# Optimization experiments

Hardware: AMD Instinct MI355X
Metric: run time of the kernel (lower is better)

Reference implementation:

```python
import jax, jax.numpy as jnp
import numpy as np

# Profile-HMM forward-backward in log space.
# inputs : (M, B, L, S) soft/one-hot observation features
# log_A  : (M, Q, Q) row-stochastic log transition matrix
# log_pi : (M, Q)    log initial distribution
# log_B  : (M, Q, S) log emission matrix

M, B, L, Q, S = 1, 64, 2048, 256, 26
EPS = 1e-16


def setup_inputs() -> dict:
    key = jax.random.key(0)
    k1, k2, k3, k4 = jax.random.split(key, 4)
    inputs = jax.random.uniform(k1, (M, B, L, S), dtype=jnp.float32)
    log_A = jax.nn.log_softmax(jax.random.normal(k2, (M, Q, Q), dtype=jnp.float32), axis=-1)
    log_pi = jax.nn.log_softmax(jax.random.normal(k3, (M, Q), dtype=jnp.float32), axis=-1)
    log_B = jax.nn.log_softmax(jax.random.normal(k4, (M, Q, S), dtype=jnp.float32), axis=-1)
    return {"inputs": inputs, "log_A": log_A, "log_pi": log_pi, "log_B": log_B}


def _forward_backward(inputs, log_A, log_pi, log_B):
    # emission probs per state: e[m,b,l,q] = sum_s inputs[m,b,l,s] * B[m,q,s]
    emit = jnp.einsum('mbls,mqs->mblq', inputs, jnp.exp(log_B))
    log_e = jnp.log(emit + EPS)
    log_e_t = jnp.moveaxis(log_e, 2, 0)  # (L, M, B, Q) time-major

    # forward recursion: alpha_t[i] = logsumexp_j(alpha_{t-1}[j] + A[j,i]) + e_t[i]
    alpha0 = log_pi[:, None, :] + log_e_t[0]  # (M, B, Q)

    def fstep(alpha, le):
        new = jax.nn.logsumexp(alpha[..., :, None] + log_A[:, None], axis=-2) + le
        return new, new

    _, alphas = jax.lax.scan(fstep, alpha0, log_e_t[1:])
    alphas = jnp.concatenate([alpha0[None], alphas], axis=0)  # (L, M, B, Q)

    # backward recursion: beta_t[i] = logsumexp_j(A[i,j] + e_{t+1}[j] + beta_{t+1}[j])
    beta_last = jnp.zeros_like(alpha0)

    def bstep(beta, le):
        new = jax.nn.logsumexp(log_A[:, None] + (le + beta)[:, :, None, :], axis=-1)
        return new, new

    _, betas = jax.lax.scan(bstep, beta_last, log_e_t[1:], reverse=True)
    betas = jnp.concatenate([betas, beta_last[None]], axis=0)  # (L, M, B, Q)

    loglik = jax.nn.logsumexp(alphas[-1], axis=-1)  # (M, B)
    post = alphas + betas - loglik[None, :, :, None]  # state posterior log probs
    return jnp.moveaxis(post, 0, 2), loglik  # (M, B, L, Q), (M, B)


def reference(inputs, log_A, log_pi, log_B):
    post, loglik = _forward_backward(inputs, log_A, log_pi, log_B)
    return post, loglik
```

## Files before the change

kernel.cpp:

```cpp
#include <hip/hip_runtime.h>

namespace {

constexpr int B = 64;
constexpr int L = 2048;
constexpr int Q = 256;
constexpr int S = 26;
constexpr float EPS = 1e-16f;
constexpr size_t POST = (size_t)B * L * Q;

typedef _Float16 f16x8 __attribute__((ext_vector_type(8)));
typedef float f32x4 __attribute__((ext_vector_type(4)));

#define MFMA16(a, b, c) __builtin_amdgcn_mfma_f32_16x16x32_f16((a), (b), (c), 0, 0, 0)

struct Smem {
  alignas(16) _Float16 vb[2][Q];
  float sh[2];
  alignas(16) float afin[Q];
};

__device__ __forceinline__ void lds_barrier() {
  asm volatile("s_waitcnt lgkmcnt(0)\n\ts_barrier" ::: "memory");
}

__device__ __forceinline__ float wave_max64(float x) {
#pragma unroll
  for (int off = 32; off > 0; off >>= 1) x = fmaxf(x, __shfl_xor(x, off, 64));
  return x;
}
__device__ __forceinline__ float wave_sum64(float x) {
#pragma unroll
  for (int off = 32; off > 0; off >>= 1) x += __shfl_xor(x, off, 64);
  return x;
}

__device__ __forceinline__ void load_emit_frags(const float* __restrict__ log_B,
                                                int c0, int c1, int g, int q,
                                                f16x8& Bh0, f16x8& Bl0,
                                                f16x8& Bh1, f16x8& Bl1) {
#pragma unroll
  for (int j = 0; j < 8; ++j) {
    const int s = g * 8 + j;
    const float v0 = (s < S) ? __expf(log_B[(size_t)(c0 + q) * S + s]) : 0.f;
    const float v1 = (s < S) ? __expf(log_B[(size_t)(c1 + q) * S + s]) : 0.f;
    const _Float16 h0 = (_Float16)v0, h1 = (_Float16)v1;
    Bh0[j] = h0; Bl0[j] = (_Float16)(v0 - (float)h0);
    Bh1[j] = h1; Bl1[j] = (_Float16)(v1 - (float)h1);
  }
}

__device__ __forceinline__ void load_row(const float* __restrict__ row, int g,
                                         bool rdl, float2* ld) {
  if (rdl) {
    const float2* r2 = (const float2*)(row + g * 8);
    ld[0] = r2[0];
    if (g < 3) { ld[1] = r2[1]; ld[2] = r2[2]; ld[3] = r2[3]; }
  }
}

__device__ __forceinline__ void cvt_row(const float2* ld, f16x8& xh, f16x8& xl) {
#pragma unroll
  for (int i = 0; i < 4; ++i) {
    const float a = ld[i].x, bb = ld[i].y;
    const _Float16 ah = (_Float16)a, bh = (_Float16)bb;
    xh[2 * i] = ah;     xl[2 * i] = (_Float16)(a - (float)ah);
    xh[2 * i + 1] = bh; xl[2 * i + 1] = (_Float16)(bb - (float)bh);
  }
}

__device__ __forceinline__ void emit_mfma(const f16x8& xh, const f16x8& xl,
                                          const f16x8& Bh0, const f16x8& Bl0,
                                          const f16x8& Bh1, const f16x8& Bl1,
                                          f32x4& E0, f32x4& E1) {
  const f32x4 Z = {0.f, 0.f, 0.f, 0.f};
  E0 = MFMA16(xh, Bl0, Z);
  E0 = MFMA16(xl, Bh0, E0);
  E0 = MFMA16(xh, Bh0, E0);
  E1 = MFMA16(xh, Bl1, Z);
  E1 = MFMA16(xl, Bh1, E1);
  E1 = MFMA16(xh, Bh1, E1);
}

__device__ __forceinline__ void matvec_mfma(const f16x8* va, const f16x8* T0,
                                            const f16x8* T1, float& x0, float& x1) {
  const f32x4 Z = {0.f, 0.f, 0.f, 0.f};
  f32x4 X0a = MFMA16(va[0], T0[0], Z);
  f32x4 X1a = MFMA16(va[0], T1[0], Z);
  f32x4 X0b = MFMA16(va[4], T0[4], Z);
  f32x4 X1b = MFMA16(va[4], T1[4], Z);
#pragma unroll
  for (int f = 1; f < 4; ++f) {
    X0a = MFMA16(va[f], T0[f], X0a);
    X1a = MFMA16(va[f], T1[f], X1a);
    X0b = MFMA16(va[f + 4], T0[f + 4], X0b);
    X1b = MFMA16(va[f + 4], T1[f + 4], X1b);
  }
  x0 = X0a[0] + X0b[0];
  x1 = X1a[0] + X1b[0];
}

__device__ __forceinline__ void read_frags(Smem& sm, int p, int g, f16x8* va) {
  const _Float16* vbp = sm.vb[p];
#pragma unroll
  for (int f = 0; f < 8; ++f) va[f] = *(const f16x8*)(vbp + f * 32 + g * 8);
}

__device__ __forceinline__ void fwd_impl(int b, const float* __restrict__ inputs,
                                         const float* __restrict__ log_A,
                                         const float* __restrict__ log_pi,
                                         const float* __restrict__ log_B,
                                         float* __restrict__ out, Smem& sm) {
  const int tid = threadIdx.x, w = tid >> 6, lane = tid & 63;
  const int g = lane >> 4, q = lane & 15;
  const int c0 = w * 32, c1 = c0 + 16;
  const bool rdl = (q == 0);
  const bool epi = (lane < 16);

  f16x8 T0[8], T1[8];
#pragma unroll
  for (int f = 0; f < 8; ++f) {
#pragma unroll
    for (int j = 0; j < 8; ++j) {
      const int k = f * 32 + g * 8 + j;
      T0[f][j] = (_Float16)__expf(log_A[(size_t)k * Q + c0 + q]);
      T1[f][j] = (_Float16)__expf(log_A[(size_t)k * Q + c1 + q]);
    }
  }
  f16x8 Bh0, Bl0, Bh1, Bl1;
  load_emit_frags(log_B, c0, c1, g, q, Bh0, Bl0, Bh1, Bl1);

  const float* __restrict__ rowbase = inputs + (size_t)b * L * S;
  float* __restrict__ post_b = out + (size_t)b * L * Q;

  float2 ld[4] = {{0.f, 0.f}, {0.f, 0.f}, {0.f, 0.f}, {0.f, 0.f}};
  f16x8 xh = {}, xl = {};
  f16x8 va[8];
#pragma unroll
  for (int f = 0; f < 8; ++f) va[f] = f16x8{};

  load_row(rowbase, g, rdl, ld);
  cvt_row(ld, xh, xl);
  f32x4 E0, E1;
  emit_mfma(xh, xl, Bh0, Bl0, Bh1, Bl1, E0, E1);
  load_row(rowbase + S, g, rdl, ld);
  float zh0 = 1.f, zh1 = 1.f, rdp_h = 0.f;
  if (epi) {
    zh0 = (E0[0] + EPS) * __expf(log_pi[c0 + lane]);
    zh1 = (E1[0] + EPS) * __expf(log_pi[c1 + lane]);
  }
  if (tid == 0) sm.sh[0] = __logf(zh0);
  lds_barrier();
  float rd_prev = sm.sh[0];
  if (epi) {
    const float sc = __expf(-rd_prev);
    sm.vb[0][c0 + lane] = (_Float16)(zh0 * sc);
    sm.vb[0][c1 + lane] = (_Float16)(zh1 * sc);
  }
  lds_barrier();

  int p = 0;
  for (int t = 1; t < L; ++t) {
    const float rd = sm.sh[p];
    if (rdl) read_frags(sm, p, g, va);
    cvt_row(ld, xh, xl);
    const int tt = (t + 1 < L) ? t + 1 : L - 1;
    load_row(rowbase + (size_t)tt * S, g, rdl, ld);
    if (epi) {
      const float a0 = __logf(zh0) + rdp_h;
      const float a1 = __logf(zh1) + rdp_h;
      post_b[(size_t)(t - 1) * Q + c0 + lane] = a0;
      post_b[(size_t)(t - 1) * Q + c1 + lane] = a1;
    }
    f32x4 E0_, E1_;
    emit_mfma(xh, xl, Bh0, Bl0, Bh1, Bl1, E0_, E1_);
    float x0, x1;
    matvec_mfma(va, T0, T1, x0, x1);
    const float gam = __expf(rd_prev - rd);
    if (epi) {
      const float e0 = E0_[0] + EPS, e1 = E1_[0] + EPS;
      const float z0 = x0 * e0, z1 = x1 * e1;
      sm.vb[p ^ 1][c0 + lane] = (_Float16)(z0 * gam);
      sm.vb[p ^ 1][c1 + lane] = (_Float16)(z1 * gam);
      if (tid == 0) sm.sh[p ^ 1] = __logf(z0) + rd_prev;
      zh0 = z0; zh1 = z1;
    }
    rdp_h = rd_prev;
    rd_prev = rd;
    lds_barrier();
    p ^= 1;
  }

  if (epi) {
    const float a0 = __logf(zh0) + rdp_h;
    const float a1 = __logf(zh1) + rdp_h;
    post_b[(size_t)(L - 1) * Q + c0 + lane] = a0;
    post_b[(size_t)(L - 1) * Q + c1 + lane] = a1;
    sm.afin[c0 + lane] = a0;
    sm.afin[c1 + lane] = a1;
  }
  lds_barrier();
  if (w == 0) {
    float4 fa = ((const float4*)sm.afin)[lane];
    float m = fmaxf(fmaxf(fa.x, fa.y), fmaxf(fa.z, fa.w));
    m = wave_max64(m);
    float ss = __expf(fa.x - m) + __expf(fa.y - m) + __expf(fa.z - m) + __expf(fa.w - m);
    ss = wave_sum64(ss);
    if (lane == 0) out[POST + b] = __logf(ss) + m;
  }
}

template <int MODE>
__device__ __forceinline__ void bwd_impl(int b, const float* __restrict__ inputs,
                                         const float* __restrict__ log_A,
                                         const float* __restrict__ log_B,
                                         float* __restrict__ out,
                                         float* __restrict__ ws, Smem& sm) {
  const int tid = threadIdx.x, w = tid >> 6, lane = tid & 63;
  const int g = lane >> 4, q = lane & 15;
  const int c0 = w * 32, c1 = c0 + 16;
  const bool rdl = (q == 0);
  const bool epi = (lane < 16);

  f16x8 T0[8], T1[8];
#pragma unroll
  for (int f = 0; f < 8; ++f) {
#pragma unroll
    for (int j = 0; j < 8; ++j) {
      const int k = f * 32 + g * 8 + j;
      T0[f][j] = (_Float16)__expf(log_A[(size_t)(c0 + q) * Q + k]);
      T1[f][j] = (_Float16)__expf(log_A[(size_t)(c1 + q) * Q + k]);
    }
  }
  f16x8 Bh0, Bl0, Bh1, Bl1;
  load_emit_frags(log_B, c0, c1, g, q, Bh0, Bl0, Bh1, Bl1);

  const float* __restrict__ rowbase = inputs + (size_t)b * L * S;
  float* __restrict__ post_b = out + (size_t)b * L * Q;
  float* __restrict__ ws_b = ws + (size_t)b * L * Q;

  float ll = 0.f, a_h0 = 0.f, a_h1 = 0.f;
  if (MODE == 1) {
    ll = out[POST + b];
    if (epi) {
      a_h0 = post_b[(size_t)(L - 1) * Q + c0 + lane];
      a_h1 = post_b[(size_t)(L - 1) * Q + c1 + lane];
    }
  }

  float2 ld[4] = {{0.f, 0.f}, {0.f, 0.f}, {0.f, 0.f}, {0.f, 0.f}};
  f16x8 xh = {}, xl = {};
  f16x8 va[8];
#pragma unroll
  for (int f = 0; f < 8; ++f) va[f] = f16x8{};

  load_row(rowbase + (size_t)(L - 1) * S, g, rdl, ld);
  cvt_row(ld, xh, xl);
  f32x4 E0, E1;
  emit_mfma(xh, xl, Bh0, Bl0, Bh1, Bl1, E0, E1);
  load_row(rowbase + (size_t)(L - 2) * S, g, rdl, ld);
  float e0i = 1.f, e1i = 1.f;
  if (epi) { e0i = E0[0] + EPS; e1i = E1[0] + EPS; }
  if (tid == 0) sm.sh[0] = __logf(e0i);
  lds_barrier();
  float rd_prev = sm.sh[0];
  if (epi) {
    const float sc = __expf(-rd_prev);
    sm.vb[0][c0 + lane] = (_Float16)(e0i * sc);
    sm.vb[0][c1 + lane] = (_Float16)(e1i * sc);
  }
  float rh0 = 1.f, rh1 = 1.f, rdp_h = 0.f;
  lds_barrier();

  int p = 0;
  for (int t = L - 2; t >= 0; --t) {
    const float rd = sm.sh[p];
    if (rdl) read_frags(sm, p, g, va);
    cvt_row(ld, xh, xl);
    const int tt = (t > 0) ? t - 1 : 0;
    load_row(rowbase + (size_t)tt * S, g, rdl, ld);
    if (epi) {
      const float b0 = __logf(rh0) + rdp_h;
      const float b1 = __logf(rh1) + rdp_h;
      if (MODE == 0) {
        ws_b[(size_t)(t + 1) * Q + c0 + lane] = b0;
        ws_b[(size_t)(t + 1) * Q + c1 + lane] = b1;
      } else {
        post_b[(size_t)(t + 1) * Q + c0 + lane] = a_h0 + b0 - ll;
        post_b[(size_t)(t + 1) * Q + c1 + lane] = a_h1 + b1 - ll;
        a_h0 = post_b[(size_t)t * Q + c0 + lane];
        a_h1 = post_b[(size_t)t * Q + c1 + lane];
      }
    }
    f32x4 E0_, E1_;
    emit_mfma(xh, xl, Bh0, Bl0, Bh1, Bl1, E0_, E1_);
    float r0, r1;
    matvec_mfma(va, T0, T1, r0, r1);
    const float gam = __expf(rd_prev - rd);
    if (epi) {
      const float e0 = E0_[0] + EPS, e1 = E1_[0] + EPS;
      const float z0 = r0 * e0, z1 = r1 * e1;
      sm.vb[p ^ 1][c0 + lane] = (_Float16)(z0 * gam);
      sm.vb[p ^ 1][c1 + lane] = (_Float16)(z1 * gam);
      if (tid == 0) sm.sh[p ^ 1] = __logf(z0) + rd_prev;
      rh0 = r0; rh1 = r1;
    }
    rdp_h = rd_prev;
    rd_prev = rd;
    lds_barrier();
    p ^= 1;
  }

  if (epi) {
    const float b0 = __logf(rh0) + rdp_h;
    const float b1 = __logf(rh1) + rdp_h;
    if (MODE == 0) {
      ws_b[c0 + lane] = b0;
      ws_b[c1 + lane] = b1;
    } else {
      post_b[c0 + lane] = a_h0 + b0 - ll;
      post_b[c1 + lane] = a_h1 + b1 - ll;
    }
  }
}

__global__ __launch_bounds__(512, 2)
void hmm_fwdbwd(const float* __restrict__ inputs, const float* __restrict__ log_A,
                const float* __restrict__ log_pi, const float* __restrict__ log_B,
                float* __restrict__ out, float* __restrict__ ws) {
  __shared__ Smem sm;
  if (blockIdx.x < B) fwd_impl(blockIdx.x, inputs, log_A, log_pi, log_B, out, sm);
  else                bwd_impl<0>(blockIdx.x - B, inputs, log_A, log_B, out, ws, sm);
}

__global__ __launch_bounds__(256)
void hmm_combine(const float* __restrict__ ws, float* __restrict__ out) {
  const size_t idx = (size_t)blockIdx.x * 256 + threadIdx.x;
  const int b = (int)(idx >> 17);
  const float ll = out[POST + b];
  float4 a = ((const float4*)out)[idx];
  const float4 be = ((const float4*)ws)[idx];
  a.x += be.x - ll;
  a.y += be.y - ll;
  a.z += be.z - ll;
  a.w += be.w - ll;
  ((float4*)out)[idx] = a;
}

__global__ __launch_bounds__(512, 2)
void hmm_fwd_only(const float* __restrict__ inputs, const float* __restrict__ log_A,
                  const float* __restrict__ log_pi, const float* __restrict__ log_B,
                  float* __restrict__ out) {
  __shared__ Smem sm;
  fwd_impl(blockIdx.x, inputs, log_A, log_pi, log_B, out, sm);
}

__global__ __launch_bounds__(512, 2)
void hmm_bwd_fused(const float* __restrict__ inputs, const float* __restrict__ log_A,
                   const float* __restrict__ log_B, float* __restrict__ out) {
  __shared__ Smem sm;
  bwd_impl<1>(blockIdx.x, inputs, log_A, log_B, out, nullptr, sm);
}

}

extern "C" void kernel_launch(void* const* d_in, const int* in_sizes, int n_in,
                              void* d_out, int out_size, void* d_ws, size_t ws_size,
                              hipStream_t stream) {
  const float* inputs = (const float*)d_in[0];
  const float* log_A  = (const float*)d_in[1];
  const float* log_pi = (const float*)d_in[2];
  const float* log_B  = (const float*)d_in[3];
  float* out = (float*)d_out;
  float* ws  = (float*)d_ws;

  if (ws_size >= POST * sizeof(float)) {
    hipLaunchKernelGGL(hmm_fwdbwd, dim3(2 * B), dim3(512), 0, stream,
                       inputs, log_A, log_pi, log_B, out, ws);
    hipLaunchKernelGGL(hmm_combine, dim3((unsigned)(POST / 4 / 256)), dim3(256), 0, stream,
                       ws, out);
  } else {
    hipLaunchKernelGGL(hmm_fwd_only, dim3(B), dim3(512), 0, stream,
                       inputs, log_A, log_pi, log_B, out);
    hipLaunchKernelGGL(hmm_bwd_fused, dim3(B), dim3(512), 0, stream,
                       inputs, log_A, log_B, out);
  }
}
```

Measured before the change: 1.743 ms.

## Use four waves per block with 64 states each and double-buffered row prefetch

Each block drops from 8 waves covering 32 states apiece to 4 waves covering 64 states, so every wave keeps four transition-matrix column tiles in registers and runs four MFMA chains per step. The goal is a cheaper per-timestep block barrier with fewer waves to synchronise, plus more independent MFMA work per wave to hide latency. The input rows are now prefetched two steps ahead through two alternating buffers, and the loop is unrolled by two. The barrier is wrapped in sched_barrier. The cost is much higher register pressure, since T alone becomes 32 f16x8 vectors, and fewer waves per CU to hide latency.

Result: slower. 1.917 ms (+10.0%).

```diff
diff --git a/kernel.cpp b/kernel.cpp
--- a/kernel.cpp
+++ b/kernel.cpp
@@ -21,7 +21,10 @@
 };
 
 __device__ __forceinline__ void lds_barrier() {
-  asm volatile("s_waitcnt lgkmcnt(0)\n\ts_barrier" ::: "memory");
+  __builtin_amdgcn_sched_barrier(0);
+  asm volatile("s_waitcnt lgkmcnt(0)");
+  __builtin_amdgcn_s_barrier();
+  __builtin_amdgcn_sched_barrier(0);
 }
 
 __device__ __forceinline__ float wave_max64(float x) {
@@ -35,27 +38,12 @@
   return x;
 }
 
-__device__ __forceinline__ void load_emit_frags(const float* __restrict__ log_B,
-                                                int c0, int c1, int g, int q,
-                                                f16x8& Bh0, f16x8& Bl0,
-                                                f16x8& Bh1, f16x8& Bl1) {
-#pragma unroll
-  for (int j = 0; j < 8; ++j) {
-    const int s = g * 8 + j;
-    const float v0 = (s < S) ? __expf(log_B[(size_t)(c0 + q) * S + s]) : 0.f;
-    const float v1 = (s < S) ? __expf(log_B[(size_t)(c1 + q) * S + s]) : 0.f;
-    const _Float16 h0 = (_Float16)v0, h1 = (_Float16)v1;
-    Bh0[j] = h0; Bl0[j] = (_Float16)(v0 - (float)h0);
-    Bh1[j] = h1; Bl1[j] = (_Float16)(v1 - (float)h1);
-  }
-}
-
-__device__ __forceinline__ void load_row(const float* __restrict__ row, int g,
+__device__ __forceinline__ void load_row(const float2* __restrict__ r2, int g,
                                          bool rdl, float2* ld) {
   if (rdl) {
-    const float2* r2 = (const float2*)(row + g * 8);
-    ld[0] = r2[0];
-    if (g < 3) { ld[1] = r2[1]; ld[2] = r2[2]; ld[3] = r2[3]; }
+    const float2* p = r2 + g * 4;
+    ld[0] = p[0];
+    if (g < 3) { ld[1] = p[1]; ld[2] = p[2]; ld[3] = p[3]; }
   }
 }
 
@@ -69,35 +57,32 @@
   }
 }
 
-__device__ __forceinline__ void emit_mfma(const f16x8& xh, const f16x8& xl,
-                                          const f16x8& Bh0, const f16x8& Bl0,
-                                          const f16x8& Bh1, const f16x8& Bl1,
-                                          f32x4& E0, f32x4& E1) {
+__device__ __forceinline__ void emit4(const f16x8& xh, const f16x8& xl,
+                                      const f16x8* Bh, const f16x8* Bl, float* e) {
   const f32x4 Z = {0.f, 0.f, 0.f, 0.f};
-  E0 = MFMA16(xh, Bl0, Z);
-  E0 = MFMA16(xl, Bh0, E0);
-  E0 = MFMA16(xh, Bh0, E0);
-  E1 = MFMA16(xh, Bl1, Z);
-  E1 = MFMA16(xl, Bh1, E1);
-  E1 = MFMA16(xh, Bh1, E1);
-}
-
-__device__ __forceinline__ void matvec_mfma(const f16x8* va, const f16x8* T0,
-                                            const f16x8* T1, float& x0, float& x1) {
+#pragma unroll
+  for (int k = 0; k < 4; ++k) {
+    f32x4 E = MFMA16(xh, Bl[k], Z);
+    E = MFMA16(xl, Bh[k], E);
+    E = MFMA16(xh, Bh[k], E);
+    e[k] = E[0] + EPS;
+  }
+}
+
+__device__ __forceinline__ void matvec4(const f16x8* va, const f16x8 (*T)[8],
+                                        float* x) {
   const f32x4 Z = {0.f, 0.f, 0.f, 0.f};
-  f32x4 X0a = MFMA16(va[0], T0[0], Z);
-  f32x4 X1a = MFMA16(va[0], T1[0], Z);
-  f32x4 X0b = MFMA16(va[4], T0[4], Z);
-  f32x4 X1b = MFMA16(va[4], T1[4], Z);
-#pragma unroll
-  for (int f = 1; f < 4; ++f) {
-    X0a = MFMA16(va[f], T0[f], X0a);
-    X1a = MFMA16(va[f], T1[f], X1a);
-    X0b = MFMA16(va[f + 4], T0[f + 4], X0b);
-    X1b = MFMA16(va[f + 4], T1[f + 4], X1b);
-  }
-  x0 = X0a[0] + X0b[0];
-  x1 = X1a[0] + X1b[0];
+#pragma unroll
+  for (int k = 0; k < 4; ++k) {
+    f32x4 Xa = MFMA16(va[0], T[k][0], Z);
+    f32x4 Xb = MFMA16(va[4], T[k][4], Z);
+#pragma unroll
+    for (int f = 1; f < 4; ++f) {
+      Xa = MFMA16(va[f], T[k][f], Xa);
+      Xb = MFMA16(va[f + 4], T[k][f + 4], Xb);
+    }
+    x[k] = Xa[0] + Xb[0];
+  }
 }
 
 __device__ __forceinline__ void read_frags(Smem& sm, int p, int g, f16x8* va) {
@@ -113,91 +98,114 @@
                                          float* __restrict__ out, Smem& sm) {
   const int tid = threadIdx.x, w = tid >> 6, lane = tid & 63;
   const int g = lane >> 4, q = lane & 15;
-  const int c0 = w * 32, c1 = c0 + 16;
+  const int cw = w * 64;
   const bool rdl = (q == 0);
   const bool epi = (lane < 16);
 
-  f16x8 T0[8], T1[8];
-#pragma unroll
-  for (int f = 0; f < 8; ++f) {
+  f16x8 T[4][8];
+#pragma unroll
+  for (int k = 0; k < 4; ++k)
+#pragma unroll
+    for (int f = 0; f < 8; ++f)
+#pragma unroll
+      for (int j = 0; j < 8; ++j)
+        T[k][f][j] =
+            (_Float16)__expf(log_A[(size_t)(f * 32 + g * 8 + j) * Q + cw + 16 * k + q]);
+
+  f16x8 Bh[4], Bl[4];
+#pragma unroll
+  for (int k = 0; k < 4; ++k)
 #pragma unroll
     for (int j = 0; j < 8; ++j) {
-      const int k = f * 32 + g * 8 + j;
-      T0[f][j] = (_Float16)__expf(log_A[(size_t)k * Q + c0 + q]);
-      T1[f][j] = (_Float16)__expf(log_A[(size_t)k * Q + c1 + q]);
-    }
-  }
-  f16x8 Bh0, Bl0, Bh1, Bl1;
-  load_emit_frags(log_B, c0, c1, g, q, Bh0, Bl0, Bh1, Bl1);
-
-  const float* __restrict__ rowbase = inputs + (size_t)b * L * S;
+      const int s = g * 8 + j;
+      const float v = (s < S) ? __expf(log_B[(size_t)(cw + 16 * k + q) * S + s]) : 0.f;
+      const _Float16 h = (_Float16)v;
+      Bh[k][j] = h;
+      Bl[k][j] = (_Float16)(v - (float)h);
+    }
+
+  const float2* __restrict__ inp2 = (const float2*)(inputs + (size_t)b * L * S);
+  const float2* __restrict__ rlast = inp2 + (size_t)(L - 1) * 13;
   float* __restrict__ post_b = out + (size_t)b * L * Q;
 
-  float2 ld[4] = {{0.f, 0.f}, {0.f, 0.f}, {0.f, 0.f}, {0.f, 0.f}};
+  float2 R0[4] = {}, P0[4] = {}, P1[4] = {};
+  load_row(inp2, g, rdl, R0);
+  load_row(inp2 + 13, g, rdl, P1);
+  load_row(inp2 + 26, g, rdl, P0);
+
   f16x8 xh = {}, xl = {};
   f16x8 va[8];
 #pragma unroll
   for (int f = 0; f < 8; ++f) va[f] = f16x8{};
 
-  load_row(rowbase, g, rdl, ld);
-  cvt_row(ld, xh, xl);
-  f32x4 E0, E1;
-  emit_mfma(xh, xl, Bh0, Bl0, Bh1, Bl1, E0, E1);
-  load_row(rowbase + S, g, rdl, ld);
-  float zh0 = 1.f, zh1 = 1.f, rdp_h = 0.f;
+  cvt_row(R0, xh, xl);
+  float e[4];
+  emit4(xh, xl, Bh, Bl, e);
+  float zh[4] = {1.f, 1.f, 1.f, 1.f};
+  float rdp_h = 0.f;
   if (epi) {
-    zh0 = (E0[0] + EPS) * __expf(log_pi[c0 + lane]);
-    zh1 = (E1[0] + EPS) * __expf(log_pi[c1 + lane]);
-  }
-  if (tid == 0) sm.sh[0] = __logf(zh0);
+#pragma unroll
+    for (int k = 0; k < 4; ++k) zh[k] = e[k] * __expf(log_pi[cw + 16 * k + lane]);
+  }
+  if (tid == 0) sm.sh[0] = __logf(zh[0]);
   lds_barrier();
   float rd_prev = sm.sh[0];
   if (epi) {
     const float sc = __expf(-rd_prev);
-    sm.vb[0][c0 + lane] = (_Float16)(zh0 * sc);
-    sm.vb[0][c1 + lane] = (_Float16)(zh1 * sc);
+#pragma unroll
+    for (int k = 0; k < 4; ++k) sm.vb[0][cw + 16 * k + lane] = (_Float16)(zh[k] * sc);
   }
   lds_barrier();
 
+  const float2* pf = inp2 + 3 * 13;
+  float* pb = post_b + cw + lane;
   int p = 0;
-  for (int t = 1; t < L; ++t) {
+
+  auto step = [&](int t, float2* Pc) {
     const float rd = sm.sh[p];
     if (rdl) read_frags(sm, p, g, va);
-    cvt_row(ld, xh, xl);
-    const int tt = (t + 1 < L) ? t + 1 : L - 1;
-    load_row(rowbase + (size_t)tt * S, g, rdl, ld);
+    cvt_row(Pc, xh, xl);
+    const float2* pu = (t + 2 < L) ? pf : rlast;
+    load_row(pu, g, rdl, Pc);
+    pf += 13;
     if (epi) {
-      const float a0 = __logf(zh0) + rdp_h;
-      const float a1 = __logf(zh1) + rdp_h;
-      post_b[(size_t)(t - 1) * Q + c0 + lane] = a0;
-      post_b[(size_t)(t - 1) * Q + c1 + lane] = a1;
-    }
-    f32x4 E0_, E1_;
-    emit_mfma(xh, xl, Bh0, Bl0, Bh1, Bl1, E0_, E1_);
-    float x0, x1;
-    matvec_mfma(va, T0, T1, x0, x1);
+#pragma unroll
+      for (int k = 0; k < 4; ++k) pb[16 * k] = __logf(zh[k]) + rdp_h;
+    }
+    pb += Q;
+    float ee[4], x[4];
+    emit4(xh, xl, Bh, Bl, ee);
+    matvec4(va, T, x);
     const float gam = __expf(rd_prev - rd);
     if (epi) {
-      const float e0 = E0_[0] + EPS, e1 = E1_[0] + EPS;
-      const float z0 = x0 * e0, z1 = x1 * e1;
-      sm.vb[p ^ 1][c0 + lane] = (_Float16)(z0 * gam);
-      sm.vb[p ^ 1][c1 + lane] = (_Float16)(z1 * gam);
-      if (tid == 0) sm.sh[p ^ 1] = __logf(z0) + rd_prev;
-      zh0 = z0; zh1 = z1;
+#pragma unroll
+      for (int k = 0; k < 4; ++k) {
+        const float z = x[k] * ee[k];
+        sm.vb[p ^ 1][cw + 16 * k + lane] = (_Float16)(z * gam);
+        zh[k] = z;
+      }
+      if (tid == 0) sm.sh[p ^ 1] = __logf(zh[0]) + rd_prev;
     }
     rdp_h = rd_prev;
     rd_prev = rd;
     lds_barrier();
     p ^= 1;
-  }
+  };
+
+  int t = 1;
+  for (; t + 1 < L; t += 2) {
+    step(t, P1);
+    step(t + 1, P0);
+  }
+  step(t, P1);
 
   if (epi) {
-    const float a0 = __logf(zh0) + rdp_h;
-    const float a1 = __logf(zh1) + rdp_h;
-    post_b[(size_t)(L - 1) * Q + c0 + lane] = a0;
-    post_b[(size_t)(L - 1) * Q + c1 + lane] = a1;
-    sm.afin[c0 + lane] = a0;
-    sm.afin[c1 + lane] = a1;
+#pragma unroll
+    for (int k = 0; k < 4; ++k) {
+      const float a = __logf(zh[k]) + rdp_h;
+      pb[16 * k] = a;
+      sm.afin[cw + 16 * k + lane] = a;
+    }
   }
   lds_barrier();
   if (w == 0) {
@@ -218,113 +226,133 @@
                                          float* __restrict__ ws, Smem& sm) {
   const int tid = threadIdx.x, w = tid >> 6, lane = tid & 63;
   const int g = lane >> 4, q = lane & 15;
-  const int c0 = w * 32, c1 = c0 + 16;
+  const int cw = w * 64;
   const bool rdl = (q == 0);
   const bool epi = (lane < 16);
 
-  f16x8 T0[8], T1[8];
-#pragma unroll
-  for (int f = 0; f < 8; ++f) {
+  f16x8 T[4][8];
+#pragma unroll
+  for (int k = 0; k < 4; ++k)
+#pragma unroll
+    for (int f = 0; f < 8; ++f)
+#pragma unroll
+      for (int j = 0; j < 8; ++j)
+        T[k][f][j] =
+            (_Float16)__expf(log_A[(size_t)(cw + 16 * k + q) * Q + f * 32 + g * 8 + j]);
+
+  f16x8 Bh[4], Bl[4];
+#pragma unroll
+  for (int k = 0; k < 4; ++k)
 #pragma unroll
     for (int j = 0; j < 8; ++j) {
-      const int k = f * 32 + g * 8 + j;
-      T0[f][j] = (_Float16)__expf(log_A[(size_t)(c0 + q) * Q + k]);
-      T1[f][j] = (_Float16)__expf(log_A[(size_t)(c1 + q) * Q + k]);
-    }
-  }
-  f16x8 Bh0, Bl0, Bh1, Bl1;
-  load_emit_frags(log_B, c0, c1, g, q, Bh0, Bl0, Bh1, Bl1);
-
-  const float* __restrict__ rowbase = inputs + (size_t)b * L * S;
+      const int s = g * 8 + j;
+      const float v = (s < S) ? __expf(log_B[(size_t)(cw + 16 * k + q) * S + s]) : 0.f;
+      const _Float16 h = (_Float16)v;
+      Bh[k][j] = h;
+      Bl[k][j] = (_Float16)(v - (float)h);
+    }
+
+  const float2* __restrict__ inp2 = (const float2*)(inputs + (size_t)b * L * S);
   float* __restrict__ post_b = out + (size_t)b * L * Q;
   float* __restrict__ ws_b = ws + (size_t)b * L * Q;
 
-  float ll = 0.f, a_h0 = 0.f, a_h1 = 0.f;
+  float ll = 0.f, a_h[4] = {0.f, 0.f, 0.f, 0.f};
   if (MODE == 1) {
     ll = out[POST + b];
     if (epi) {
-      a_h0 = post_b[(size_t)(L - 1) * Q + c0 + lane];
-      a_h1 = post_b[(size_t)(L - 1) * Q + c1 + lane];
-    }
-  }
-
-  float2 ld[4] = {{0.f, 0.f}, {0.f, 0.f}, {0.f, 0.f}, {0.f, 0.f}};
+#pragma unroll
+      for (int k = 0; k < 4; ++k) a_h[k] = post_b[(size_t)(L - 1) * Q + cw + 16 * k + lane];
+    }
+  }
+
+  float2 R0[4] = {}, P0[4] = {}, P1[4] = {};
+  load_row(inp2 + (size_t)(L - 1) * 13, g, rdl, R0);
+  load_row(inp2 + (size_t)(L - 2) * 13, g, rdl, P0);
+  load_row(inp2 + (size_t)(L - 3) * 13, g, rdl, P1);
+
   f16x8 xh = {}, xl = {};
   f16x8 va[8];
 #pragma unroll
   for (int f = 0; f < 8; ++f) va[f] = f16x8{};
 
-  load_row(rowbase + (size_t)(L - 1) * S, g, rdl, ld);
-  cvt_row(ld, xh, xl);
-  f32x4 E0, E1;
-  emit_mfma(xh, xl, Bh0, Bl0, Bh1, Bl1, E0, E1);
-  load_row(rowbase + (size_t)(L - 2) * S, g, rdl, ld);
-  float e0i = 1.f, e1i = 1.f;
-  if (epi) { e0i = E0[0] + EPS; e1i = E1[0] + EPS; }
-  if (tid == 0) sm.sh[0] = __logf(e0i);
+  cvt_row(R0, xh, xl);
+  float e[4];
+  emit4(xh, xl, Bh, Bl, e);
+  if (tid == 0) sm.sh[0] = __logf(e[0]);
   lds_barrier();
   float rd_prev = sm.sh[0];
   if (epi) {
     const float sc = __expf(-rd_prev);
-    sm.vb[0][c0 + lane] = (_Float16)(e0i * sc);
-    sm.vb[0][c1 + lane] = (_Float16)(e1i * sc);
-  }
-  float rh0 = 1.f, rh1 = 1.f, rdp_h = 0.f;
+#pragma unroll
+    for (int k = 0; k < 4; ++k) sm.vb[0][cw + 16 * k + lane] = (_Float16)(e[k] * sc);
+  }
+  float rh[4] = {1.f, 1.f, 1.f, 1.f};
+  float rdp_h = 0.f;
   lds_barrier();
 
+  const float2* pf = inp2 + (size_t)(L - 4) * 13;
+  float* wp = ws_b + (size_t)(L - 1) * Q + cw + lane;
+  float* pp = post_b + (size_t)(L - 1) * Q + cw + lane;
   int p = 0;
-  for (int t = L - 2; t >= 0; --t) {
+
+  auto step = [&](int t, float2* Pc) {
     const float rd = sm.sh[p];
     if (rdl) read_frags(sm, p, g, va);
-    cvt_row(ld, xh, xl);
-    const int tt = (t > 0) ? t - 1 : 0;
-    load_row(rowbase + (size_t)tt * S, g, rdl, ld);
+    cvt_row(Pc, xh, xl);
+    const float2* pu = (t >= 2) ? pf : inp2;
+    load_row(pu, g, rdl, Pc);
+    pf -= 13;
     if (epi) {
-      const float b0 = __logf(rh0) + rdp_h;
-      const float b1 = __logf(rh1) + rdp_h;
       if (MODE == 0) {
-        ws_b[(size_t)(t + 1) * Q + c0 + lane] = b0;
-        ws_b[(size_t)(t + 1) * Q + c1 + lane] = b1;
+#pragma unroll
+        for (int k = 0; k < 4; ++k) wp[16 * k] = __logf(rh[k]) + rdp_h;
       } else {
-        post_b[(size_t)(t + 1) * Q + c0 + lane] = a_h0 + b0 - ll;
-        post_b[(size_t)(t + 1) * Q + c1 + lane] = a_h1 + b1 - ll;
-        a_h0 = post_b[(size_t)t * Q + c0 + lane];
-        a_h1 = post_b[(size_t)t * Q + c1 + lane];
+#pragma unroll
+        for (int k = 0; k < 4; ++k) pp[16 * k] = a_h[k] + __logf(rh[k]) + rdp_h - ll;
+#pragma unroll
+        for (int k = 0; k < 4; ++k) a_h[k] = (pp - Q)[16 * k];
       }
     }
-    f32x4 E0_, E1_;
-    emit_mfma(xh, xl, Bh0, Bl0, Bh1, Bl1, E0_, E1_);
-    float r0, r1;
-    matvec_mfma(va, T0, T1, r0, r1);
+    wp -= Q;
+    pp -= Q;
+    float ee[4], x[4];
+    emit4(xh, xl, Bh, Bl, ee);
+    matvec4(va, T, x);
     const float gam = __expf(rd_prev - rd);
     if (epi) {
-      const float e0 = E0_[0] + EPS, e1 = E1_[0] + EPS;
-      const float z0 = r0 * e0, z1 = r1 * e1;
-      sm.vb[p ^ 1][c0 + lane] = (_Float16)(z0 * gam);
-      sm.vb[p ^ 1][c1 + lane] = (_Float16)(z1 * gam);
-      if (tid == 0) sm.sh[p ^ 1] = __logf(z0) + rd_prev;
-      rh0 = r0; rh1 = r1;
+#pragma unroll
+      for (int k = 0; k < 4; ++k) {
+        const float z = x[k] * ee[k];
+        sm.vb[p ^ 1][cw + 16 * k + lane] = (_Float16)(z * gam);
+        rh[k] = x[k];
+      }
+      if (tid == 0) sm.sh[p ^ 1] = __logf(x[0] * ee[0]) + rd_prev;
     }
     rdp_h = rd_prev;
     rd_prev = rd;
     lds_barrier();
     p ^= 1;
-  }
+  };
+
+  int t = L - 2;
+  for (; t >= 1; t -= 2) {
+    step(t, P0);
+    step(t - 1, P1);
+  }
+  step(0, P0);
 
   if (epi) {
-    const float b0 = __logf(rh0) + rdp_h;
-    const float b1 = __logf(rh1) + rdp_h;
     if (MODE == 0) {
-      ws_b[c0 + lane] = b0;
-      ws_b[c1 + lane] = b1;
+#pragma unroll
+      for (int k = 0; k < 4; ++k) wp[16 * k] = __logf(rh[k]) + rdp_h;
     } else {
-      post_b[c0 + lane] = a_h0 + b0 - ll;
-      post_b[c1 + lane] = a_h1 + b1 - ll;
-    }
-  }
-}
-
-__global__ __launch_bounds__(512, 2)
+#pragma unroll
+      for (int k = 0; k < 4; ++k) pp[16 * k] = a_h[k] + __logf(rh[k]) + rdp_h - ll;
+    }
+  }
+}
+
+__global__ __launch_bounds__(256, 1)
 void hmm_fwdbwd(const float* __restrict__ inputs, const float* __restrict__ log_A,
                 const float* __restrict__ log_pi, const float* __restrict__ log_B,
                 float* __restrict__ out, float* __restrict__ ws) {
@@ -347,7 +375,7 @@
   ((float4*)out)[idx] = a;
 }
 
-__global__ __launch_bounds__(512, 2)
+__global__ __launch_bounds__(256, 1)
 void hmm_fwd_only(const float* __restrict__ inputs, const float* __restrict__ log_A,
                   const float* __restrict__ log_pi, const float* __restrict__ log_B,
                   float* __restrict__ out) {
@@ -355,7 +383,7 @@
   fwd_impl(blockIdx.x, inputs, log_A, log_pi, log_B, out, sm);
 }
 
-__global__ __launch_bounds__(512, 2)
+__global__ __launch_bounds__(256, 1)
 void hmm_bwd_fused(const float* __restrict__ inputs, const float* __restrict__ log_A,
                    const float* __restrict__ log_B, float* __restrict__ out) {
   __shared__ Smem sm;
@@ -375,14 +403,14 @@
   float* ws  = (float*)d_ws;
 
   if (ws_size >= POST * sizeof(float)) {
-    hipLaunchKernelGGL(hmm_fwdbwd, dim3(2 * B), dim3(512), 0, stream,
+    hipLaunchKernelGGL(hmm_fwdbwd, dim3(2 * B), dim3(256), 0, stream,
                        inputs, log_A, log_pi, log_B, out, ws);
     hipLaunchKernelGGL(hmm_combine, dim3((unsigned)(POST / 4 / 256)), dim3(256), 0, stream,
                        ws, out);
   } else {
-    hipLaunchKernelGGL(hmm_fwd_only, dim3(B), dim3(512), 0, stream,
+    hipLaunchKernelGGL(hmm_fwd_only, dim3(B), dim3(256), 0, stream,
                        inputs, log_A, log_pi, log_B, out);
-    hipLaunchKernelGGL(hmm_bwd_fused, dim3(B), dim3(512), 0, stream,
+    hipLaunchKernelGGL(hmm_bwd_fused, dim3(B), dim3(256), 0, stream,
                        inputs, log_A, log_B, out);
   }
 }
```
